# Performance work log

Measured on AMD Instinct MI355X. Metric: run time of the kernel, lower is better.

The kernel has to match this reference:

```python
import jax, jax.numpy as jnp
import numpy as np

B, T, D_IN, H = 2048, 240, 180, 90


def setup_inputs() -> dict:
    key = jax.random.key(0)
    k1, k2, k3, k4, k5 = jax.random.split(key, 5)
    s = 1.0 / np.sqrt(H)  # torch LSTMCell init scale
    return {
        "x": jax.random.normal(k1, (B, 3, 60, 240), dtype=jnp.float32),
        "W_ih": jax.random.uniform(k2, (4 * H, D_IN), dtype=jnp.float32, minval=-s, maxval=s),
        "W_hh": jax.random.uniform(k3, (4 * H, H), dtype=jnp.float32, minval=-s, maxval=s),
        "b_ih": jax.random.uniform(k4, (4 * H,), dtype=jnp.float32, minval=-s, maxval=s),
        "b_hh": jax.random.uniform(k5, (4 * H,), dtype=jnp.float32, minval=-s, maxval=s),
    }


def reference(x, W_ih, W_hh, b_ih, b_hh):
    # (B, 3, 60, 240) -> (B, 240, 3, 60) -> (B, 240, 180)
    b = x.shape[0]
    xt = jnp.transpose(x, (0, 3, 1, 2)).reshape(b, T, D_IN)
    # NOTE: the torch module calls LSTMCell without carrying state, so h0=c0=0
    # at EVERY timestep; the W_hh contribution is identically zero and all
    # timesteps are independent -> one batched GEMM over (B*T).
    gates = jnp.einsum("bti,gi->btg", xt, W_ih) + b_ih + b_hh  # (B, T, 4H)
    i_g, f_g, g_g, o_g = jnp.split(gates, 4, axis=-1)  # torch gate order i,f,g,o
    c = jax.nn.sigmoid(i_g) * jnp.tanh(g_g)  # f_g * c_prev = 0
    h = jax.nn.sigmoid(o_g) * jnp.tanh(c)
    return jax.nn.sigmoid(h)  # (B, T, H)
```

## Files before the change

### kernel.cpp

```cpp
#include <hip/hip_runtime.h>


#define B_SZ 2048
#define T_SZ 240
#define K_SZ 180
#define H_SZ 90
#define KP   192
#define TC   48
#define NC   5
#define TPC  3

#define WS_W_BYTES 110592
#define WS_B_OFF   110592

typedef __bf16 bf16x8 __attribute__((ext_vector_type(8)));
typedef float  f32x4  __attribute__((ext_vector_type(4)));

__device__ __forceinline__ float sigmoidf_(float x) {
    return __builtin_amdgcn_rcpf(1.0f + __expf(-x));
}
__device__ __forceinline__ float tanhf_(float x) {
    return 1.0f - 2.0f * __builtin_amdgcn_rcpf(__expf(2.0f * x) + 1.0f);
}

__device__ __forceinline__ int fsw(int t) {
    return (t & 7) ^ (((t >> 3) & 1) << 2);
}
__device__ __forceinline__ int aidx(int t, int k) {
    int g    = k >> 3;
    int slot = (g & ~7) | ((g & 7) ^ fsw(t & 15));
    return t * KP + (slot << 3) + (k & 7);
}

__global__ __launch_bounds__(384) void prepack_kernel(
    const float* __restrict__ W_ih,
    const float* __restrict__ b_ih,
    const float* __restrict__ b_hh,
    void* __restrict__ ws)
{
    __bf16* wp = (__bf16*)ws;
    float*  bp = (float*)((char*)ws + WS_B_OFF);
    const int gb[3] = {0, 180, 270};

    const int bid = blockIdx.x;
    const int tid = threadIdx.x;
    if (bid < 18) {
        const int g  = bid / 6;
        const int ks = bid % 6;
        const int w  = tid >> 6;
        const int l  = tid & 63;
        const int q  = l >> 4;
        const int n  = l & 15;
        const int h  = w * 16 + n;
        bf16x8 f;
        #pragma unroll
        for (int j = 0; j < 8; ++j) {
            int k = ks * 32 + q * 8 + j;
            float v = (h < H_SZ && k < K_SZ) ? W_ih[(size_t)(gb[g] + h) * K_SZ + k] : 0.0f;
            f[j] = (__bf16)v;
        }
        *(bf16x8*)(wp + (size_t)(((g * 6 + ks) * 6 + w) * 64 + l) * 8) = f;
    } else {
        if (tid < 288) {
            int g = tid / 96, hh = tid % 96;
            bp[g * 96 + hh] = (hh < H_SZ) ? (b_ih[gb[g] + hh] + b_hh[gb[g] + hh]) : 0.0f;
        }
    }
}

__device__ __forceinline__ void stage_chunk(
    const float* __restrict__ xb, __bf16* __restrict__ dst, int c, int tid)
{
    #pragma unroll
    for (int p = 0; p < 6; ++p) {
        int u = tid + p * 384;
        if (p < 5 || u < 2160) {
            int k  = u / 12;
            int t4 = u - k * 12;
            const f32x4 v = *(const f32x4*)(xb + k * T_SZ + c * TC + t4 * 4);
            #pragma unroll
            for (int i = 0; i < 4; ++i)
                dst[aidx(t4 * 4 + i, k)] = (__bf16)v[i];
        }
    }
}

__global__ __launch_bounds__(384, 3) void lstm_fused_kernel(
    const float* __restrict__ x,
    const void*  __restrict__ ws,
    float* __restrict__ out)
{
    __shared__ __align__(16) __bf16 aBuf[2][TC * KP];

    const int b    = blockIdx.x;
    const int tid  = threadIdx.x;
    const int wave = tid >> 6;
    const int lane = tid & 63;
    const int q    = lane >> 4;
    const int n    = lane & 15;
    const int h    = wave * 16 + n;
    const bool hv  = (h < H_SZ);

    const bf16x8* wp = (const bf16x8*)ws;
    bf16x8 bfrag[3][6];
    #pragma unroll
    for (int g = 0; g < 3; ++g)
        #pragma unroll
        for (int ks = 0; ks < 6; ++ks)
            bfrag[g][ks] = wp[((g * 6 + ks) * 6 + wave) * 64 + lane];

    const float* bp = (const float*)((const char*)ws + WS_B_OFF);
    const float bias_i = bp[0 * 96 + h];
    const float bias_g = bp[1 * 96 + h];
    const float bias_o = bp[2 * 96 + h];

    const float* xb = x   + (size_t)b * (K_SZ * T_SZ);
    float*       ob = out + (size_t)b * (T_SZ * H_SZ);

    for (int e = tid; e < 2 * TC * 12; e += 384) {
        int buf = e / (TC * 12);
        int r   = e - buf * (TC * 12);
        int t   = r / 12;
        int k   = K_SZ + (r - (r / 12) * 12);
        aBuf[buf][aidx(t, k)] = (__bf16)0.0f;
    }

    stage_chunk(xb, aBuf[0], 0, tid);
    __syncthreads();

    int cur = 0;
    #pragma unroll 1
    for (int c = 0; c < NC; ++c) {
        if (c + 1 < NC)
            stage_chunk(xb, aBuf[cur ^ 1], c + 1, tid);

        const __bf16* ab = aBuf[cur];
        #pragma unroll
        for (int tt = 0; tt < TPC; ++tt) {
            f32x4 acc0 = {0.f, 0.f, 0.f, 0.f};
            f32x4 acc1 = {0.f, 0.f, 0.f, 0.f};
            f32x4 acc2 = {0.f, 0.f, 0.f, 0.f};
            #pragma unroll
            for (int ks = 0; ks < 6; ++ks) {
                int g    = ks * 4 + q;
                int slot = (g & ~7) | ((g & 7) ^ fsw(n));
                bf16x8 a = *(const bf16x8*)(ab + (tt * 16 + n) * KP + (slot << 3));
                acc0 = __builtin_amdgcn_mfma_f32_16x16x32_bf16(a, bfrag[0][ks], acc0, 0, 0, 0);
                acc1 = __builtin_amdgcn_mfma_f32_16x16x32_bf16(a, bfrag[1][ks], acc1, 0, 0, 0);
                acc2 = __builtin_amdgcn_mfma_f32_16x16x32_bf16(a, bfrag[2][ks], acc2, 0, 0, 0);
            }
            if (hv) {
                const int tg = c * TC + tt * 16 + q * 4;
                #pragma unroll
                for (int e = 0; e < 4; ++e) {
                    float gi = acc0[e] + bias_i;
                    float gg = acc1[e] + bias_g;
                    float go = acc2[e] + bias_o;
                    float cc = sigmoidf_(gi) * tanhf_(gg);
                    float hh = sigmoidf_(go) * tanhf_(cc);
                    ob[(size_t)(tg + e) * H_SZ + h] = sigmoidf_(hh);
                }
            }
        }
        __syncthreads();
        cur ^= 1;
    }
}

extern "C" void kernel_launch(void* const* d_in, const int* in_sizes, int n_in,
                              void* d_out, int out_size, void* d_ws, size_t ws_size,
                              hipStream_t stream) {
    const float* x    = (const float*)d_in[0];
    const float* W_ih = (const float*)d_in[1];
    const float* b_ih = (const float*)d_in[3];
    const float* b_hh = (const float*)d_in[4];
    float* out = (float*)d_out;

    prepack_kernel<<<dim3(19), dim3(384), 0, stream>>>(W_ih, b_ih, b_hh, d_ws);
    lstm_fused_kernel<<<dim3(B_SZ), dim3(384), 0, stream>>>(x, d_ws, out);
}
```

Measured before the change: 647.1 us.

## Split each batch row into three single-shot time tiles with wider staging

Each block now handles one 80-timestep slice of a batch row instead of looping over five double-buffered 48-step chunks. The grid grows threefold and occupancy is raised to 5 blocks per CU. Staging reads four K rows at once and writes 4-wide bf16 vectors under a new swizzle, and weight fragments are loaded per k-step rather than kept resident. This drops the per-chunk barriers and pipeline bookkeeping in favour of more concurrent blocks hiding latency, at the cost of more accumulator registers and reloading weights from L2.

Result: slower. 662.9 us (+2.4%).

```diff
diff --git a/kernel.cpp b/kernel.cpp
--- a/kernel.cpp
+++ b/kernel.cpp
@@ -6,14 +6,14 @@
 #define K_SZ 180
 #define H_SZ 90
 #define KP   192
-#define TC   48
-#define NC   5
-#define TPC  3
+#define TB   80
+#define NP   3
+#define NTT  5
 
-#define WS_W_BYTES 110592
-#define WS_B_OFF   110592
+#define WS_B_OFF 110592
 
 typedef __bf16 bf16x8 __attribute__((ext_vector_type(8)));
+typedef __bf16 bf16x4 __attribute__((ext_vector_type(4)));
 typedef float  f32x4  __attribute__((ext_vector_type(4)));
 
 __device__ __forceinline__ float sigmoidf_(float x) {
@@ -23,13 +23,11 @@
     return 1.0f - 2.0f * __builtin_amdgcn_rcpf(__expf(2.0f * x) + 1.0f);
 }
 
-__device__ __forceinline__ int fsw(int t) {
-    return (t & 7) ^ (((t >> 3) & 1) << 2);
+__device__ __forceinline__ int skey(int t) {
+    return (2 * (t + (t >> 4))) & 14;
 }
-__device__ __forceinline__ int aidx(int t, int k) {
-    int g    = k >> 3;
-    int slot = (g & ~7) | ((g & 7) ^ fsw(t & 15));
-    return t * KP + (slot << 3) + (k & 7);
+__device__ __forceinline__ int sgran(int g, int t) {
+    return (g & ~15) | ((g ^ skey(t)) & 15);
 }
 
 __global__ __launch_bounds__(384) void prepack_kernel(
@@ -68,31 +66,18 @@
     }
 }
 
-__device__ __forceinline__ void stage_chunk(
-    const float* __restrict__ xb, __bf16* __restrict__ dst, int c, int tid)
-{
-    #pragma unroll
-    for (int p = 0; p < 6; ++p) {
-        int u = tid + p * 384;
-        if (p < 5 || u < 2160) {
-            int k  = u / 12;
-            int t4 = u - k * 12;
-            const f32x4 v = *(const f32x4*)(xb + k * T_SZ + c * TC + t4 * 4);
-            #pragma unroll
-            for (int i = 0; i < 4; ++i)
-                dst[aidx(t4 * 4 + i, k)] = (__bf16)v[i];
-        }
-    }
-}
-
-__global__ __launch_bounds__(384, 3) void lstm_fused_kernel(
+__global__ __launch_bounds__(384, 5) void lstm_fused_kernel(
     const float* __restrict__ x,
     const void*  __restrict__ ws,
     float* __restrict__ out)
 {
-    __shared__ __align__(16) __bf16 aBuf[2][TC * KP];
+    __shared__ __align__(16) __bf16 aBuf[TB * KP];
 
-    const int b    = blockIdx.x;
+    const int bid  = blockIdx.x;
+    const int b    = bid / NP;
+    const int part = bid - b * NP;
+    const int t0   = part * TB;
+
     const int tid  = threadIdx.x;
     const int wave = tid >> 6;
     const int lane = tid & 63;
@@ -101,69 +86,81 @@
     const int h    = wave * 16 + n;
     const bool hv  = (h < H_SZ);
 
+    const float* xb = x + (size_t)b * (K_SZ * T_SZ) + t0;
+
+    if (tid < TB * 3) {
+        int t  = tid / 3;
+        int gz = 45 + (tid - (tid / 3) * 3);
+        *(unsigned long long*)(aBuf + t * KP + sgran(gz, t) * 4) = 0ull;
+    }
+
+    #pragma unroll
+    for (int p = 0; p < 3; ++p) {
+        int u = tid + p * 384;
+        if (p < 2 || u < 900) {
+            int k4 = u / 20;
+            int t4 = u - k4 * 20;
+            const float* src = xb + (k4 * 4) * T_SZ + t4 * 4;
+            f32x4 r0 = *(const f32x4*)(src);
+            f32x4 r1 = *(const f32x4*)(src + T_SZ);
+            f32x4 r2 = *(const f32x4*)(src + 2 * T_SZ);
+            f32x4 r3 = *(const f32x4*)(src + 3 * T_SZ);
+            #pragma unroll
+            for (int j = 0; j < 4; ++j) {
+                int t = t4 * 4 + j;
+                bf16x4 w;
+                w[0] = (__bf16)r0[j]; w[1] = (__bf16)r1[j];
+                w[2] = (__bf16)r2[j]; w[3] = (__bf16)r3[j];
+                *(bf16x4*)(aBuf + t * KP + sgran(k4, t) * 4) = w;
+            }
+        }
+    }
+    __syncthreads();
+
     const bf16x8* wp = (const bf16x8*)ws;
-    bf16x8 bfrag[3][6];
+
+    f32x4 acc[NTT][3];
     #pragma unroll
-    for (int g = 0; g < 3; ++g)
+    for (int tt = 0; tt < NTT; ++tt)
         #pragma unroll
-        for (int ks = 0; ks < 6; ++ks)
-            bfrag[g][ks] = wp[((g * 6 + ks) * 6 + wave) * 64 + lane];
+        for (int g = 0; g < 3; ++g)
+            acc[tt][g] = (f32x4){0.f, 0.f, 0.f, 0.f};
+
+    #pragma unroll
+    for (int ks = 0; ks < 6; ++ks) {
+        bf16x8 b0 = wp[((0 * 6 + ks) * 6 + wave) * 64 + lane];
+        bf16x8 b1 = wp[((1 * 6 + ks) * 6 + wave) * 64 + lane];
+        bf16x8 b2 = wp[((2 * 6 + ks) * 6 + wave) * 64 + lane];
+        #pragma unroll
+        for (int tt = 0; tt < NTT; ++tt) {
+            int t = tt * 16 + n;
+            int g = ks * 8 + 2 * q;
+            bf16x8 a = *(const bf16x8*)(aBuf + t * KP + sgran(g, t) * 4);
+            acc[tt][0] = __builtin_amdgcn_mfma_f32_16x16x32_bf16(a, b0, acc[tt][0], 0, 0, 0);
+            acc[tt][1] = __builtin_amdgcn_mfma_f32_16x16x32_bf16(a, b1, acc[tt][1], 0, 0, 0);
+            acc[tt][2] = __builtin_amdgcn_mfma_f32_16x16x32_bf16(a, b2, acc[tt][2], 0, 0, 0);
+        }
+    }
 
     const float* bp = (const float*)((const char*)ws + WS_B_OFF);
     const float bias_i = bp[0 * 96 + h];
     const float bias_g = bp[1 * 96 + h];
     const float bias_o = bp[2 * 96 + h];
+    float* ob = out + (size_t)b * (T_SZ * H_SZ) + (size_t)t0 * H_SZ;
 
-    const float* xb = x   + (size_t)b * (K_SZ * T_SZ);
-    float*       ob = out + (size_t)b * (T_SZ * H_SZ);
-
-    for (int e = tid; e < 2 * TC * 12; e += 384) {
-        int buf = e / (TC * 12);
-        int r   = e - buf * (TC * 12);
-        int t   = r / 12;
-        int k   = K_SZ + (r - (r / 12) * 12);
-        aBuf[buf][aidx(t, k)] = (__bf16)0.0f;
-    }
-
-    stage_chunk(xb, aBuf[0], 0, tid);
-    __syncthreads();
-
-    int cur = 0;
-    #pragma unroll 1
-    for (int c = 0; c < NC; ++c) {
-        if (c + 1 < NC)
-            stage_chunk(xb, aBuf[cur ^ 1], c + 1, tid);
-
-        const __bf16* ab = aBuf[cur];
+    if (hv) {
         #pragma unroll
-        for (int tt = 0; tt < TPC; ++tt) {
-            f32x4 acc0 = {0.f, 0.f, 0.f, 0.f};
-            f32x4 acc1 = {0.f, 0.f, 0.f, 0.f};
-            f32x4 acc2 = {0.f, 0.f, 0.f, 0.f};
+        for (int tt = 0; tt < NTT; ++tt) {
             #pragma unroll
-            for (int ks = 0; ks < 6; ++ks) {
-                int g    = ks * 4 + q;
-                int slot = (g & ~7) | ((g & 7) ^ fsw(n));
-                bf16x8 a = *(const bf16x8*)(ab + (tt * 16 + n) * KP + (slot << 3));
-                acc0 = __builtin_amdgcn_mfma_f32_16x16x32_bf16(a, bfrag[0][ks], acc0, 0, 0, 0);
-                acc1 = __builtin_amdgcn_mfma_f32_16x16x32_bf16(a, bfrag[1][ks], acc1, 0, 0, 0);
-                acc2 = __builtin_amdgcn_mfma_f32_16x16x32_bf16(a, bfrag[2][ks], acc2, 0, 0, 0);
-            }
-            if (hv) {
-                const int tg = c * TC + tt * 16 + q * 4;
-                #pragma unroll
-                for (int e = 0; e < 4; ++e) {
-                    float gi = acc0[e] + bias_i;
-                    float gg = acc1[e] + bias_g;
-                    float go = acc2[e] + bias_o;
-                    float cc = sigmoidf_(gi) * tanhf_(gg);
-                    float hh = sigmoidf_(go) * tanhf_(cc);
-                    ob[(size_t)(tg + e) * H_SZ + h] = sigmoidf_(hh);
-                }
+            for (int e = 0; e < 4; ++e) {
+                float gi = acc[tt][0][e] + bias_i;
+                float gg = acc[tt][1][e] + bias_g;
+                float go = acc[tt][2][e] + bias_o;
+                float cc = sigmoidf_(gi) * tanhf_(gg);
+                float hh = sigmoidf_(go) * tanhf_(cc);
+                ob[(size_t)(tt * 16 + q * 4 + e) * H_SZ + h] = sigmoidf_(hh);
             }
         }
-        __syncthreads();
-        cur ^= 1;
     }
 }
 
@@ -177,5 +174,5 @@
     float* out = (float*)d_out;
 
     prepack_kernel<<<dim3(19), dim3(384), 0, stream>>>(W_ih, b_ih, b_hh, d_ws);
-    lstm_fused_kernel<<<dim3(B_SZ), dim3(384), 0, stream>>>(x, d_ws, out);
+    lstm_fused_kernel<<<dim3(B_SZ * NP), dim3(384), 0, stream>>>(x, d_ws, out);
 }
```
